# Kernel optimization log

Measured on AMD Instinct MI355X. Metric: run time of the kernel, lower is better.

The kernel has to match this reference:

```python
import jax, jax.numpy as jnp
import numpy as np


def _gru(x, h, Wx, Wh, b):
    # Keras-convention GRUCell (reset_after=False): h' = z*h + (1-z)*hh
    D = h.shape[-1]
    g = x @ Wx + b                       # [N, 3D]
    xz, xr, xh = g[..., :D], g[..., D:2 * D], g[..., 2 * D:]
    z = jax.nn.sigmoid(xz + h @ Wh[:, :D])
    r = jax.nn.sigmoid(xr + h @ Wh[:, D:2 * D])
    hh = jnp.tanh(xh + (r * h) @ Wh[:, 2 * D:])
    return z * h + (1.0 - z) * hh


def setup_inputs():
    key = jax.random.key(0)
    ks = jax.random.split(key, 12)
    num_links, num_quests, num_paths = 20000, 200, 100
    total_paths = num_quests * num_paths
    L, link_dim, path_dim, T = 8, 64, 64, 8
    s = 0.05
    links = jax.random.randint(ks[0], (total_paths * L,), 0, num_links)
    paths = jnp.repeat(jnp.arange(total_paths), L)   # sorted, as segment_sum requires
    seqs = jnp.tile(jnp.arange(L), total_paths)      # hop position within each path
    return {
        "link_capacity": jax.random.uniform(ks[1], (num_links,), jnp.float32),
        "traffic": jax.random.uniform(ks[2], (total_paths,), jnp.float32),
        "links": links, "paths": paths, "seqs": seqs,
        "pWx": jax.random.normal(ks[3], (link_dim, 3 * path_dim), jnp.float32) * s,
        "pWh": jax.random.normal(ks[4], (path_dim, 3 * path_dim), jnp.float32) * s,
        "pb": jnp.zeros((3 * path_dim,), jnp.float32),
        "eWx": jax.random.normal(ks[5], (path_dim, 3 * link_dim), jnp.float32) * s,
        "eWh": jax.random.normal(ks[6], (link_dim, 3 * link_dim), jnp.float32) * s,
        "eb": jnp.zeros((3 * link_dim,), jnp.float32),
        "W1": jax.random.normal(ks[7], (path_dim, 256), jnp.float32) * s,
        "b1": jnp.zeros((256,), jnp.float32),
        "W2": jax.random.normal(ks[8], (256, 256), jnp.float32) * s,
        "b2": jnp.zeros((256,), jnp.float32),
        "W3": jax.random.normal(ks[9], (256, 1), jnp.float32) * s,
        "b3": jnp.zeros((1,), jnp.float32),
        "T": T, "num_quests": num_quests, "num_paths": num_paths,
    }


def reference(link_capacity, traffic, links, paths, seqs,
              pWx, pWh, pb, eWx, eWh, eb, W1, b1, W2, b2, W3, b3,
              T, num_quests, num_paths):
    num_links = link_capacity.shape[0]
    total_paths = num_quests * num_paths
    link_dim = eWh.shape[0]
    path_dim = pWh.shape[0]
    E = links.shape[0]
    L = E // total_paths                      # static max path length (fixed-length paths)

    # per-path lengths (tf.math.segment_sum of ones over sorted `paths`)
    lens = jax.ops.segment_sum(jnp.ones_like(paths), paths, num_segments=total_paths)

    link_state = jnp.concatenate(
        [link_capacity[:, None], jnp.zeros((num_links, link_dim - 1), link_capacity.dtype)], axis=1)
    path_state = jnp.concatenate(
        [traffic[:total_paths, None], jnp.zeros((total_paths, path_dim - 1), traffic.dtype)], axis=1)

    for _ in range(T):
        h_tild = link_state[links]                                     # gather: [E, link_dim]
        link_inputs = jnp.zeros((total_paths, L, link_dim), h_tild.dtype)
        link_inputs = link_inputs.at[paths, seqs].set(h_tild)          # scatter_nd
        xs = jnp.transpose(link_inputs, (1, 0, 2))                     # [L, P, link_dim]

        def step(h, xt):
            x, t = xt
            mask = (t < lens)[:, None]
            h_new = _gru(x, h, pWx, pWh, pb)
            h = jnp.where(mask, h_new, h)                              # freeze past seq end
            out = jnp.where(mask, h, jnp.zeros_like(h))                # dynamic_rnn zeros tail
            return h, out

        path_state, outputs = jax.lax.scan(step, path_state, (xs, jnp.arange(L)))
        m = outputs[seqs, paths]                                       # gather_nd: [E, path_dim]
        m = jax.ops.segment_sum(m, links, num_segments=num_links)      # unsorted_segment_sum
        link_state = _gru(m, link_state, eWx, eWh, eb)                 # edge GRU update

    # readout (module calls it with training=True -> dropout active; fixed masks here)
    k1, k2 = jax.random.split(jax.random.key(1))
    h = jax.nn.selu(path_state @ W1 + b1)
    h = jnp.where(jax.random.bernoulli(k1, 0.5, h.shape), h / 0.5, 0.0)
    h = jax.nn.selu(h @ W2 + b2)
    h = jnp.where(jax.random.bernoulli(k2, 0.5, h.shape), h / 0.5, 0.0)
    r = jax.nn.relu(h @ W3 + b3)
    return r.reshape(num_quests, num_paths)
```

## Files before the change

### kernel.cpp

```cpp
#include <hip/hip_runtime.h>
#include <cstdint>

#define NLINKS 20000
#define NPATHS 20000
#define LSEQ   8
#define TITER  8
#define DD     64
#define GW     192
#define NEDGE  (NPATHS * LSEQ)
#define NB     ((NPATHS + 63) / 64)

__device__ static inline void softbar() {
  asm volatile("s_waitcnt lgkmcnt(0)" ::: "memory");
  __builtin_amdgcn_s_barrier();
  asm volatile("" ::: "memory");
}

__host__ __device__ static inline uint32_t rotl32(uint32_t x, unsigned r) {
  return (x << r) | (x >> (32u - r));
}

__host__ __device__ static inline void threefry2x32(uint32_t k0, uint32_t k1,
                                                    uint32_t c0, uint32_t c1,
                                                    uint32_t& o0, uint32_t& o1) {
  uint32_t ks0 = k0, ks1 = k1, ks2 = k0 ^ k1 ^ 0x1BD11BDAu;
  uint32_t x0 = c0 + ks0, x1 = c1 + ks1;
#define TF_R(r) { x0 += x1; x1 = rotl32(x1, r); x1 ^= x0; }
  TF_R(13) TF_R(15) TF_R(26) TF_R(6)  x0 += ks1; x1 += ks2 + 1u;
  TF_R(17) TF_R(29) TF_R(16) TF_R(24) x0 += ks2; x1 += ks0 + 2u;
  TF_R(13) TF_R(15) TF_R(26) TF_R(6)  x0 += ks0; x1 += ks1 + 3u;
  TF_R(17) TF_R(29) TF_R(16) TF_R(24) x0 += ks1; x1 += ks2 + 4u;
  TF_R(13) TF_R(15) TF_R(26) TF_R(6)  x0 += ks2; x1 += ks0 + 5u;
#undef TF_R
  o0 = x0; o1 = x1;
}

__device__ static inline bool bern_keep(uint32_t key0, uint32_t key1, uint32_t j) {
  uint32_t o0, o1;
  threefry2x32(key0, key1, 0u, j, o0, o1);
  uint32_t bits = o0 ^ o1;
  float u = __uint_as_float((bits >> 9) | 0x3f800000u) - 1.0f;
  return u < 0.5f;
}

__device__ static inline float sigmoidf_(float x) { return 1.0f / (1.0f + expf(-x)); }
__device__ static inline float seluf_(float x) {
  const float sc = 1.0507009873554805f;
  const float al = 1.6732632423543772f;
  return x > 0.0f ? sc * x : sc * al * expm1f(x);
}

__global__ void init_gather_kernel(const float* __restrict__ cap,
                                   const float* __restrict__ traffic,
                                   float* __restrict__ link_state,
                                   float* __restrict__ seq_h,
                                   int* __restrict__ counts) {
  int i = blockIdx.x * blockDim.x + threadIdx.x;
  if (i < NLINKS * DD)
    link_state[i] = ((i & 63) == 0) ? cap[i >> 6] : 0.0f;
  if (i < NPATHS * DD) {
    int p = i >> 6, j = i & 63;
    seq_h[(p * LSEQ + (LSEQ - 1)) * DD + j] = (j == 0) ? traffic[p] : 0.0f;
  }
  if (i < NLINKS) counts[i] = 0;
}

__global__ void csr_hist_kernel(const int* __restrict__ links,
                                int* __restrict__ counts) {
  int e = blockIdx.x * blockDim.x + threadIdx.x;
  if (e < NEDGE) atomicAdd(&counts[links[e]], 1);
}

__global__ __launch_bounds__(1024, 1) void csr_scan_kernel(
    const int* __restrict__ counts,
    int* __restrict__ row_start,
    int* __restrict__ cursor) {
  __shared__ int sc[1024];
  const int i = threadIdx.x;
  const int base = i * 20;
  int s = 0;
  for (int j = 0; j < 20; ++j) {
    int r = base + j;
    if (r < NLINKS) s += counts[r];
  }
  sc[i] = s;
  __syncthreads();
  for (int off = 1; off < 1024; off <<= 1) {
    int v = (i >= off) ? sc[i - off] : 0;
    __syncthreads();
    sc[i] += v;
    __syncthreads();
  }
  int run = sc[i] - s;
  for (int j = 0; j < 20; ++j) {
    int r = base + j;
    if (r < NLINKS) {
      row_start[r] = run;
      cursor[r] = run;
      run += counts[r];
    }
  }
}

__global__ void csr_fill_kernel(const int* __restrict__ links,
                                int* __restrict__ cursor,
                                int* __restrict__ edges) {
  int e = blockIdx.x * blockDim.x + threadIdx.x;
  if (e < NEDGE) {
    int l = links[e];
    int pos = atomicAdd(&cursor[l], 1);
    edges[pos] = e;
  }
}

__global__ __launch_bounds__(512, 4) void gx_kernel(
    const float* __restrict__ link_state,
    const float* __restrict__ Wx,
    const float* __restrict__ bias,
    float* __restrict__ gx) {
  __shared__ float ls_s[64][65];

  const int tid  = threadIdx.x;
  const int lane = tid & 63;
  const int w    = __builtin_amdgcn_readfirstlane(tid >> 6);
  const int l0   = blockIdx.x * 64;

  for (int i = tid; i < 1024; i += 512) {
    int p = i >> 4, c = i & 15;
    int lr = min(l0 + p, NLINKS - 1);
    float4 v = reinterpret_cast<const float4*>(link_state)[lr * 16 + c];
    ls_s[p][c * 4 + 0] = v.x; ls_s[p][c * 4 + 1] = v.y;
    ls_s[p][c * 4 + 2] = v.z; ls_s[p][c * 4 + 3] = v.w;
  }

  const int c0 = w * 24;
  float acc[24];
#pragma unroll
  for (int jj = 0; jj < 24; ++jj) acc[jj] = bias[c0 + jj];
  softbar();

#pragma unroll 4
  for (int k = 0; k < DD; ++k) {
    float xk = ls_s[lane][k];
    const float* wxp = &Wx[k * GW + c0];
#pragma unroll
    for (int jj = 0; jj < 24; ++jj)
      acc[jj] = fmaf(xk, wxp[jj], acc[jj]);
  }

  if (l0 + lane < NLINKS) {
    float* dst = &gx[(size_t)(l0 + lane) * GW + c0];
#pragma unroll
    for (int s = 0; s < 6; ++s) {
      float4 v = make_float4(acc[s * 4 + 0], acc[s * 4 + 1],
                             acc[s * 4 + 2], acc[s * 4 + 3]);
      reinterpret_cast<float4*>(dst)[s] = v;
    }
  }
}

__global__ __launch_bounds__(1024, 8) void path_gru_v9_kernel(
    const float* __restrict__ gx,
    float* __restrict__ seq_h,
    const int* __restrict__ links,
    const float* __restrict__ Wh) {
  __shared__ float h_s[64][65];
  __shared__ float z_s[64][65];
  __shared__ float r_s[64][65];

  const int tid  = threadIdx.x;
  const int lane = tid & 63;
  const int w    = __builtin_amdgcn_readfirstlane(tid >> 6);
  const int p0   = blockIdx.x * 64;

  {
    int p = tid >> 4, c = tid & 15;
    int pr = min(p0 + p, NPATHS - 1);
    float4 v = reinterpret_cast<const float4*>(seq_h)[(pr * LSEQ + 7) * 16 + c];
    h_s[p][c * 4 + 0] = v.x; h_s[p][c * 4 + 1] = v.y;
    h_s[p][c * 4 + 2] = v.z; h_s[p][c * 4 + 3] = v.w;
  }

  const int ab0 = w * 8;
  const int cc0 = 128 + w * 4;
  const int hc0 = w * 4;
  const int prow = min(p0 + lane, NPATHS - 1);
  const float4* gx4 = reinterpret_cast<const float4*>(gx);

  float4 gz0, gz1, gc0;
  {
    int li = links[prow * LSEQ + 0];
    const float4* g = gx4 + (size_t)li * (GW / 4);
    gz0 = g[ab0 / 4]; gz1 = g[ab0 / 4 + 1]; gc0 = g[cc0 / 4];
  }
  softbar();

  for (int t = 0; t < LSEQ; ++t) {
    if (t > 0) {
      int p = tid >> 4, c = tid & 15;
      if (p0 + p < NPATHS) {
        float4 v = make_float4(h_s[p][c * 4 + 0], h_s[p][c * 4 + 1],
                               h_s[p][c * 4 + 2], h_s[p][c * 4 + 3]);
        reinterpret_cast<float4*>(seq_h)[((p0 + p) * LSEQ + (t - 1)) * 16 + c] = v;
      }
    }

    float aB[8];
#pragma unroll
    for (int jj = 0; jj < 8; ++jj) aB[jj] = 0.0f;
#pragma unroll 4
    for (int k = 0; k < DD; ++k) {
      float hk = h_s[lane][k];
      const float* whp = &Wh[k * GW + ab0];
#pragma unroll
      for (int jj = 0; jj < 8; ++jj)
        aB[jj] = fmaf(hk, whp[jj], aB[jj]);
    }

    float gzf[8] = {gz0.x, gz0.y, gz0.z, gz0.w, gz1.x, gz1.y, gz1.z, gz1.w};
    if (w < 8) {
#pragma unroll
      for (int jj = 0; jj < 8; ++jj)
        z_s[lane][ab0 + jj] = sigmoidf_(gzf[jj] + aB[jj]);
    } else {
#pragma unroll
      for (int jj = 0; jj < 8; ++jj) {
        int hj = ab0 - 64 + jj;
        float r = sigmoidf_(gzf[jj] + aB[jj]);
        r_s[lane][hj] = r * h_s[lane][hj];
      }
    }
    softbar();

    int li_n = (t < LSEQ - 1) ? links[prow * LSEQ + t + 1] : 0;

    float aC[4];
#pragma unroll
    for (int jj = 0; jj < 4; ++jj) aC[jj] = 0.0f;
#pragma unroll 4
    for (int k = 0; k < DD; ++k) {
      float rhk = r_s[lane][k];
      const float* whc = &Wh[k * GW + cc0];
#pragma unroll
      for (int jj = 0; jj < 4; ++jj)
        aC[jj] = fmaf(rhk, whc[jj], aC[jj]);
    }
    float gcf[4] = {gc0.x, gc0.y, gc0.z, gc0.w};
#pragma unroll
    for (int jj = 0; jj < 4; ++jj) {
      int j = hc0 + jj;
      float z    = z_s[lane][j];
      float hold = h_s[lane][j];
      float hh = tanhf(gcf[jj] + aC[jj]);
      h_s[lane][j] = z * hold + (1.0f - z) * hh;
    }

    if (t < LSEQ - 1) {
      const float4* g = gx4 + (size_t)li_n * (GW / 4);
      gz0 = g[ab0 / 4]; gz1 = g[ab0 / 4 + 1]; gc0 = g[cc0 / 4];
    }
    softbar();
  }

  {
    int p = tid >> 4, c = tid & 15;
    if (p0 + p < NPATHS) {
      float4 v = make_float4(h_s[p][c * 4 + 0], h_s[p][c * 4 + 1],
                             h_s[p][c * 4 + 2], h_s[p][c * 4 + 3]);
      reinterpret_cast<float4*>(seq_h)[((p0 + p) * LSEQ + 7) * 16 + c] = v;
    }
  }
}

__global__ __launch_bounds__(1024, 8) void link_gru_v11_kernel(
    float* __restrict__ link_state,
    const float* __restrict__ seq_h,
    const int* __restrict__ row_start,
    const int* __restrict__ row_end,
    const int* __restrict__ edges,
    const float* __restrict__ Wx,
    const float* __restrict__ Wh,
    const float* __restrict__ bias,
    const float* __restrict__ pWx,
    const float* __restrict__ pb,
    float* __restrict__ gx_out) {
  __shared__ float h_s[64][65];
  __shared__ float x_s[64][65];
  __shared__ float r_s[64][65];

  const int tid  = threadIdx.x;
  const int lane = tid & 63;
  const int w    = __builtin_amdgcn_readfirstlane(tid >> 6);
  const int l0   = blockIdx.x * 64;

  {
    int p = tid >> 4, c = tid & 15;
    float4 hv = make_float4(0.f, 0.f, 0.f, 0.f);
    float4 xv = make_float4(0.f, 0.f, 0.f, 0.f);
    if (l0 + p < NLINKS) {
      hv = reinterpret_cast<const float4*>(link_state)[(l0 + p) * 16 + c];
      const float4* s4 = reinterpret_cast<const float4*>(seq_h);
      int rs = row_start[l0 + p], re = row_end[l0 + p];
      int ii = rs;
      for (; ii + 4 <= re; ii += 4) {
        int e0 = edges[ii + 0], e1 = edges[ii + 1];
        int e2 = edges[ii + 2], e3 = edges[ii + 3];
        float4 v0 = s4[e0 * 16 + c], v1 = s4[e1 * 16 + c];
        float4 v2 = s4[e2 * 16 + c], v3 = s4[e3 * 16 + c];
        xv.x += v0.x + v1.x + v2.x + v3.x;
        xv.y += v0.y + v1.y + v2.y + v3.y;
        xv.z += v0.z + v1.z + v2.z + v3.z;
        xv.w += v0.w + v1.w + v2.w + v3.w;
      }
      for (; ii < re; ++ii) {
        int e = edges[ii];
        float4 v = s4[e * 16 + c];
        xv.x += v.x; xv.y += v.y; xv.z += v.z; xv.w += v.w;
      }
    }
    h_s[p][c * 4 + 0] = hv.x; h_s[p][c * 4 + 1] = hv.y;
    h_s[p][c * 4 + 2] = hv.z; h_s[p][c * 4 + 3] = hv.w;
    x_s[p][c * 4 + 0] = xv.x; x_s[p][c * 4 + 1] = xv.y;
    x_s[p][c * 4 + 2] = xv.z; x_s[p][c * 4 + 3] = xv.w;
  }

  const int ab0 = w * 8;
  const int cc0 = 128 + w * 4;
  const int hc0 = w * 4;

  float bab[8], bcc[4];
#pragma unroll
  for (int jj = 0; jj < 8; ++jj) bab[jj] = bias[ab0 + jj];
#pragma unroll
  for (int jj = 0; jj < 4; ++jj) bcc[jj] = bias[cc0 + jj];

  softbar();

  float aA[8], aB[8], cA[4];
#pragma unroll
  for (int jj = 0; jj < 8; ++jj) { aA[jj] = bab[jj]; aB[jj] = 0.0f; }
#pragma unroll
  for (int jj = 0; jj < 4; ++jj) cA[jj] = bcc[jj];
#pragma unroll 4
  for (int k = 0; k < DD; ++k) {
    float xk = x_s[lane][k];
    float hk = h_s[lane][k];
    const float* wxp = &Wx[k * GW + ab0];
    const float* whp = &Wh[k * GW + ab0];
    const float* wxc = &Wx[k * GW + cc0];
#pragma unroll
    for (int jj = 0; jj < 8; ++jj) {
      aA[jj] = fmaf(xk, wxp[jj], aA[jj]);
      aB[jj] = fmaf(hk, whp[jj], aB[jj]);
    }
#pragma unroll
    for (int jj = 0; jj < 4; ++jj)
      cA[jj] = fmaf(xk, wxc[jj], cA[jj]);
  }
  softbar();

  if (w < 8) {
#pragma unroll
    for (int jj = 0; jj < 8; ++jj)
      x_s[lane][ab0 + jj] = sigmoidf_(aA[jj] + aB[jj]);
  } else {
#pragma unroll
    for (int jj = 0; jj < 8; ++jj) {
      int hj = ab0 - 64 + jj;
      float r = sigmoidf_(aA[jj] + aB[jj]);
      r_s[lane][hj] = r * h_s[lane][hj];
    }
  }
  softbar();

  float aC[4];
#pragma unroll
  for (int jj = 0; jj < 4; ++jj) aC[jj] = 0.0f;
#pragma unroll 4
  for (int k = 0; k < DD; ++k) {
    float rhk = r_s[lane][k];
    const float* whc = &Wh[k * GW + cc0];
#pragma unroll
    for (int jj = 0; jj < 4; ++jj)
      aC[jj] = fmaf(rhk, whc[jj], aC[jj]);
  }
  {
    float o[4];
#pragma unroll
    for (int jj = 0; jj < 4; ++jj) {
      int j = hc0 + jj;
      float z    = x_s[lane][j];
      float hold = h_s[lane][j];
      float hh = tanhf(cA[jj] + aC[jj]);
      o[jj] = z * hold + (1.0f - z) * hh;
      x_s[lane][j] = o[jj];
    }
    if (l0 + lane < NLINKS) {
      reinterpret_cast<float4*>(&link_state[(size_t)(l0 + lane) * DD + hc0])[0]
          = make_float4(o[0], o[1], o[2], o[3]);
    }
  }
  softbar();

  {
    const int g0 = w * 12;
    float ga[12];
#pragma unroll
    for (int jj = 0; jj < 12; ++jj) ga[jj] = pb[g0 + jj];
#pragma unroll 4
    for (int k = 0; k < DD; ++k) {
      float hk = x_s[lane][k];
      const float* wxp = &pWx[k * GW + g0];
#pragma unroll
      for (int jj = 0; jj < 12; ++jj)
        ga[jj] = fmaf(hk, wxp[jj], ga[jj]);
    }
    if (l0 + lane < NLINKS) {
      float* dst = &gx_out[(size_t)(l0 + lane) * GW + g0];
#pragma unroll
      for (int s = 0; s < 3; ++s)
        reinterpret_cast<float4*>(dst)[s] =
            make_float4(ga[s * 4 + 0], ga[s * 4 + 1], ga[s * 4 + 2], ga[s * 4 + 3]);
    }
  }
}

__global__ __launch_bounds__(1024, 8) void mlp_v9_kernel(
    const float4* __restrict__ ps4, int rs4,
    const float* __restrict__ W1, const float* __restrict__ b1,
    const float* __restrict__ W2, const float* __restrict__ b2,
    const float* __restrict__ W3, const float* __restrict__ b3,
    float* __restrict__ out,
    uint32_t k1a, uint32_t k1b, uint32_t k2a, uint32_t k2b) {
  __shared__ float hraw[64 * 257];
  __shared__ float part_s[64][17];

  const int tid  = threadIdx.x;
  const int lane = tid & 63;
  const int w    = __builtin_amdgcn_readfirstlane(tid >> 6);
  const int p0   = blockIdx.x * 64;
  const int c0   = w * 16;

  {
    int p = tid >> 4, c = tid & 15;
    int pr = min(p0 + p, NPATHS - 1);
    float4 v = ps4[(size_t)pr * rs4 + c];
    hraw[p * 65 + c * 4 + 0] = v.x; hraw[p * 65 + c * 4 + 1] = v.y;
    hraw[p * 65 + c * 4 + 2] = v.z; hraw[p * 65 + c * 4 + 3] = v.w;
  }

  float acc[16];
#pragma unroll
  for (int j = 0; j < 16; ++j) acc[j] = b1[c0 + j];
  softbar();

  const uint32_t base = (uint32_t)(p0 + lane) * 256u + (uint32_t)c0;

#pragma unroll 4
  for (int k = 0; k < DD; ++k) {
    float pk = hraw[lane * 65 + k];
    const float* wp = &W1[k * 256 + c0];
#pragma unroll
    for (int j = 0; j < 16; ++j) acc[j] = fmaf(pk, wp[j], acc[j]);
  }
  softbar();

#pragma unroll
  for (int j = 0; j < 16; ++j) {
    float v = seluf_(acc[j]);
    bool keep = bern_keep(k1a, k1b, base + (uint32_t)j);
    hraw[lane * 257 + c0 + j] = keep ? v * 2.0f : 0.0f;
  }
  softbar();

#pragma unroll
  for (int j = 0; j < 16; ++j) acc[j] = b2[c0 + j];
#pragma unroll 4
  for (int k = 0; k < 256; ++k) {
    float hk = hraw[lane * 257 + k];
    const float* wp = &W2[k * 256 + c0];
#pragma unroll
    for (int j = 0; j < 16; ++j) acc[j] = fmaf(hk, wp[j], acc[j]);
  }

  {
    float s = 0.0f;
#pragma unroll
    for (int j = 0; j < 16; ++j) {
      float v = seluf_(acc[j]);
      bool keep = bern_keep(k2a, k2b, base + (uint32_t)j);
      float h2 = keep ? v * 2.0f : 0.0f;
      s = fmaf(h2, W3[c0 + j], s);
    }
    part_s[lane][w] = s;
  }
  softbar();

  if (w == 0) {
    float t = b3[0];
#pragma unroll
    for (int ww = 0; ww < 16; ++ww) t += part_s[lane][ww];
    if (p0 + lane < NPATHS) out[p0 + lane] = t > 0.0f ? t : 0.0f;
  }
}

extern "C" void kernel_launch(void* const* d_in, const int* in_sizes, int n_in,
                              void* d_out, int out_size, void* d_ws, size_t ws_size,
                              hipStream_t stream) {
  const float* cap     = (const float*)d_in[0];
  const float* traffic = (const float*)d_in[1];
  const int*   links   = (const int*)d_in[2];
  const float* pWx = (const float*)d_in[5];
  const float* pWh = (const float*)d_in[6];
  const float* pb  = (const float*)d_in[7];
  const float* eWx = (const float*)d_in[8];
  const float* eWh = (const float*)d_in[9];
  const float* eb  = (const float*)d_in[10];
  const float* W1  = (const float*)d_in[11];
  const float* b1  = (const float*)d_in[12];
  const float* W2  = (const float*)d_in[13];
  const float* b2  = (const float*)d_in[14];
  const float* W3  = (const float*)d_in[15];
  const float* b3  = (const float*)d_in[16];
  float* out = (float*)d_out;

  uint32_t k1a, k1b, k2a, k2b;
  threefry2x32(0u, 1u, 0u, 0u, k1a, k1b);
  threefry2x32(0u, 1u, 0u, 1u, k2a, k2b);

  const size_t n_link = (size_t)NLINKS * DD;
  const size_t n_seq  = (size_t)NPATHS * LSEQ * DD;
  const size_t n_gx   = (size_t)NLINKS * GW;

  float* link_state = (float*)d_ws;
  float* seq_h      = link_state + n_link;
  float* gx         = seq_h + n_seq;
  int*   counts     = (int*)(gx + n_gx);
  int*   row_start  = counts + NLINKS;
  int*   cursor     = row_start + NLINKS;
  int*   edges      = cursor + NLINKS;

  init_gather_kernel<<<(NLINKS * DD + 255) / 256, 256, 0, stream>>>(
      cap, traffic, link_state, seq_h, counts);
  csr_hist_kernel<<<(NEDGE + 255) / 256, 256, 0, stream>>>(links, counts);
  csr_scan_kernel<<<1, 1024, 0, stream>>>(counts, row_start, cursor);
  csr_fill_kernel<<<(NEDGE + 255) / 256, 256, 0, stream>>>(links, cursor, edges);

  gx_kernel<<<NB, 512, 0, stream>>>(link_state, pWx, pb, gx);

  for (int it = 0; it < TITER; ++it) {
    path_gru_v9_kernel<<<NB, 1024, 0, stream>>>(gx, seq_h, links, pWh);
    link_gru_v11_kernel<<<NB, 1024, 0, stream>>>(link_state, seq_h,
                                                 row_start, cursor, edges,
                                                 eWx, eWh, eb,
                                                 pWx, pb, gx);
  }
  mlp_v9_kernel<<<NB, 1024, 0, stream>>>(
      (const float4*)seq_h + 7 * 16, LSEQ * 16,
      W1, b1, W2, b2, W3, b3, out, k1a, k1b, k2a, k2b);
}
```

Baseline: 1.450 ms.

## Store path GRU outputs in CSR order so link aggregation reads contiguously

After: 1.462 ms. No clear change (+0.8%).

```diff
diff --git a/kernel.cpp b/kernel.cpp
--- a/kernel.cpp
+++ b/kernel.cpp
@@ -50,21 +50,6 @@
   return x > 0.0f ? sc * x : sc * al * expm1f(x);
 }
 
-__global__ void init_gather_kernel(const float* __restrict__ cap,
-                                   const float* __restrict__ traffic,
-                                   float* __restrict__ link_state,
-                                   float* __restrict__ seq_h,
-                                   int* __restrict__ counts) {
-  int i = blockIdx.x * blockDim.x + threadIdx.x;
-  if (i < NLINKS * DD)
-    link_state[i] = ((i & 63) == 0) ? cap[i >> 6] : 0.0f;
-  if (i < NPATHS * DD) {
-    int p = i >> 6, j = i & 63;
-    seq_h[(p * LSEQ + (LSEQ - 1)) * DD + j] = (j == 0) ? traffic[p] : 0.0f;
-  }
-  if (i < NLINKS) counts[i] = 0;
-}
-
 __global__ void csr_hist_kernel(const int* __restrict__ links,
                                 int* __restrict__ counts) {
   int e = blockIdx.x * blockDim.x + threadIdx.x;
@@ -102,14 +87,29 @@
   }
 }
 
-__global__ void csr_fill_kernel(const int* __restrict__ links,
-                                int* __restrict__ cursor,
-                                int* __restrict__ edges) {
+__global__ void csr_fill_pos_kernel(const int* __restrict__ links,
+                                    int* __restrict__ cursor,
+                                    int* __restrict__ csr_pos) {
   int e = blockIdx.x * blockDim.x + threadIdx.x;
   if (e < NEDGE) {
     int l = links[e];
     int pos = atomicAdd(&cursor[l], 1);
-    edges[pos] = e;
+    csr_pos[e] = pos;
+  }
+}
+
+__global__ void init_gather2_kernel(const float* __restrict__ cap,
+                                    const float* __restrict__ traffic,
+                                    const int* __restrict__ csr_pos,
+                                    float* __restrict__ link_state,
+                                    float* __restrict__ seq_h) {
+  int i = blockIdx.x * blockDim.x + threadIdx.x;
+  if (i < NLINKS * DD)
+    link_state[i] = ((i & 63) == 0) ? cap[i >> 6] : 0.0f;
+  if (i < NPATHS * DD) {
+    int p = i >> 6, j = i & 63;
+    int row = csr_pos[p * LSEQ + (LSEQ - 1)];
+    seq_h[row * DD + j] = (j == 0) ? traffic[p] : 0.0f;
   }
 }
 
@@ -159,10 +159,11 @@
   }
 }
 
-__global__ __launch_bounds__(1024, 8) void path_gru_v9_kernel(
+__global__ __launch_bounds__(1024, 8) void path_gru_v12_kernel(
     const float* __restrict__ gx,
     float* __restrict__ seq_h,
     const int* __restrict__ links,
+    const int* __restrict__ csr_pos,
     const float* __restrict__ Wh) {
   __shared__ float h_s[64][65];
   __shared__ float z_s[64][65];
@@ -176,7 +177,8 @@
   {
     int p = tid >> 4, c = tid & 15;
     int pr = min(p0 + p, NPATHS - 1);
-    float4 v = reinterpret_cast<const float4*>(seq_h)[(pr * LSEQ + 7) * 16 + c];
+    int row = csr_pos[pr * LSEQ + 7];
+    float4 v = reinterpret_cast<const float4*>(seq_h)[row * 16 + c];
     h_s[p][c * 4 + 0] = v.x; h_s[p][c * 4 + 1] = v.y;
     h_s[p][c * 4 + 2] = v.z; h_s[p][c * 4 + 3] = v.w;
   }
@@ -199,9 +201,10 @@
     if (t > 0) {
       int p = tid >> 4, c = tid & 15;
       if (p0 + p < NPATHS) {
+        int row = csr_pos[(p0 + p) * LSEQ + (t - 1)];
         float4 v = make_float4(h_s[p][c * 4 + 0], h_s[p][c * 4 + 1],
                                h_s[p][c * 4 + 2], h_s[p][c * 4 + 3]);
-        reinterpret_cast<float4*>(seq_h)[((p0 + p) * LSEQ + (t - 1)) * 16 + c] = v;
+        reinterpret_cast<float4*>(seq_h)[row * 16 + c] = v;
       }
     }
 
@@ -232,7 +235,12 @@
     }
     softbar();
 
-    int li_n = (t < LSEQ - 1) ? links[prow * LSEQ + t + 1] : 0;
+    float4 ngz0, ngz1, ngc0;
+    if (t < LSEQ - 1) {
+      int li_n = links[prow * LSEQ + t + 1];
+      const float4* g = gx4 + (size_t)li_n * (GW / 4);
+      ngz0 = g[ab0 / 4]; ngz1 = g[ab0 / 4 + 1]; ngc0 = g[cc0 / 4];
+    }
 
     float aC[4];
 #pragma unroll
@@ -255,29 +263,26 @@
       h_s[lane][j] = z * hold + (1.0f - z) * hh;
     }
 
-    if (t < LSEQ - 1) {
-      const float4* g = gx4 + (size_t)li_n * (GW / 4);
-      gz0 = g[ab0 / 4]; gz1 = g[ab0 / 4 + 1]; gc0 = g[cc0 / 4];
-    }
+    if (t < LSEQ - 1) { gz0 = ngz0; gz1 = ngz1; gc0 = ngc0; }
     softbar();
   }
 
   {
     int p = tid >> 4, c = tid & 15;
     if (p0 + p < NPATHS) {
+      int row = csr_pos[(p0 + p) * LSEQ + 7];
       float4 v = make_float4(h_s[p][c * 4 + 0], h_s[p][c * 4 + 1],
                              h_s[p][c * 4 + 2], h_s[p][c * 4 + 3]);
-      reinterpret_cast<float4*>(seq_h)[((p0 + p) * LSEQ + 7) * 16 + c] = v;
-    }
-  }
-}
-
-__global__ __launch_bounds__(1024, 8) void link_gru_v11_kernel(
+      reinterpret_cast<float4*>(seq_h)[row * 16 + c] = v;
+    }
+  }
+}
+
+__global__ __launch_bounds__(1024, 8) void link_gru_v12_kernel(
     float* __restrict__ link_state,
     const float* __restrict__ seq_h,
     const int* __restrict__ row_start,
     const int* __restrict__ row_end,
-    const int* __restrict__ edges,
     const float* __restrict__ Wx,
     const float* __restrict__ Wh,
     const float* __restrict__ bias,
@@ -303,18 +308,17 @@
       int rs = row_start[l0 + p], re = row_end[l0 + p];
       int ii = rs;
       for (; ii + 4 <= re; ii += 4) {
-        int e0 = edges[ii + 0], e1 = edges[ii + 1];
-        int e2 = edges[ii + 2], e3 = edges[ii + 3];
-        float4 v0 = s4[e0 * 16 + c], v1 = s4[e1 * 16 + c];
-        float4 v2 = s4[e2 * 16 + c], v3 = s4[e3 * 16 + c];
+        float4 v0 = s4[(size_t)(ii + 0) * 16 + c];
+        float4 v1 = s4[(size_t)(ii + 1) * 16 + c];
+        float4 v2 = s4[(size_t)(ii + 2) * 16 + c];
+        float4 v3 = s4[(size_t)(ii + 3) * 16 + c];
         xv.x += v0.x + v1.x + v2.x + v3.x;
         xv.y += v0.y + v1.y + v2.y + v3.y;
         xv.z += v0.z + v1.z + v2.z + v3.z;
         xv.w += v0.w + v1.w + v2.w + v3.w;
       }
       for (; ii < re; ++ii) {
-        int e = edges[ii];
-        float4 v = s4[e * 16 + c];
+        float4 v = s4[(size_t)ii * 16 + c];
         xv.x += v.x; xv.y += v.y; xv.z += v.z; xv.w += v.w;
       }
     }
@@ -425,8 +429,9 @@
   }
 }
 
-__global__ __launch_bounds__(1024, 8) void mlp_v9_kernel(
-    const float4* __restrict__ ps4, int rs4,
+__global__ __launch_bounds__(1024, 8) void mlp_v10_kernel(
+    const float* __restrict__ seq_h,
+    const int* __restrict__ csr_pos,
     const float* __restrict__ W1, const float* __restrict__ b1,
     const float* __restrict__ W2, const float* __restrict__ b2,
     const float* __restrict__ W3, const float* __restrict__ b3,
@@ -444,7 +449,8 @@
   {
     int p = tid >> 4, c = tid & 15;
     int pr = min(p0 + p, NPATHS - 1);
-    float4 v = ps4[(size_t)pr * rs4 + c];
+    int row = csr_pos[pr * LSEQ + 7];
+    float4 v = reinterpret_cast<const float4*>(seq_h)[row * 16 + c];
     hraw[p * 65 + c * 4 + 0] = v.x; hraw[p * 65 + c * 4 + 1] = v.y;
     hraw[p * 65 + c * 4 + 2] = v.z; hraw[p * 65 + c * 4 + 3] = v.w;
   }
@@ -538,24 +544,27 @@
   int*   counts     = (int*)(gx + n_gx);
   int*   row_start  = counts + NLINKS;
   int*   cursor     = row_start + NLINKS;
-  int*   edges      = cursor + NLINKS;
-
-  init_gather_kernel<<<(NLINKS * DD + 255) / 256, 256, 0, stream>>>(
-      cap, traffic, link_state, seq_h, counts);
+  int*   csr_pos    = cursor + NLINKS;
+
+  hipMemsetAsync(counts, 0, NLINKS * sizeof(int), stream);
   csr_hist_kernel<<<(NEDGE + 255) / 256, 256, 0, stream>>>(links, counts);
   csr_scan_kernel<<<1, 1024, 0, stream>>>(counts, row_start, cursor);
-  csr_fill_kernel<<<(NEDGE + 255) / 256, 256, 0, stream>>>(links, cursor, edges);
+  csr_fill_pos_kernel<<<(NEDGE + 255) / 256, 256, 0, stream>>>(links, cursor,
+                                                               csr_pos);
+  init_gather2_kernel<<<(NLINKS * DD + 255) / 256, 256, 0, stream>>>(
+      cap, traffic, csr_pos, link_state, seq_h);
 
   gx_kernel<<<NB, 512, 0, stream>>>(link_state, pWx, pb, gx);
 
   for (int it = 0; it < TITER; ++it) {
-    path_gru_v9_kernel<<<NB, 1024, 0, stream>>>(gx, seq_h, links, pWh);
-    link_gru_v11_kernel<<<NB, 1024, 0, stream>>>(link_state, seq_h,
-                                                 row_start, cursor, edges,
+    path_gru_v12_kernel<<<NB, 1024, 0, stream>>>(gx, seq_h, links, csr_pos,
+                                                 pWh);
+    link_gru_v12_kernel<<<NB, 1024, 0, stream>>>(link_state, seq_h,
+                                                 row_start, cursor,
                                                  eWx, eWh, eb,
                                                  pWx, pb, gx);
   }
-  mlp_v9_kernel<<<NB, 1024, 0, stream>>>(
-      (const float4*)seq_h + 7 * 16, LSEQ * 16,
+  mlp_v10_kernel<<<NB, 1024, 0, stream>>>(
+      seq_h, csr_pos,
       W1, b1, W2, b2, W3, b3, out, k1a, k1b, k2a, k2b);
 }
```
